# Optimization experiments

Measured on AMD Instinct MI355X. Metric: run time of the kernel, lower is better.

## Reference

```python
import jax, jax.numpy as jnp
import numpy as np


def setup_inputs() -> dict:
    key = jax.random.key(0)
    k1, k2, k3 = jax.random.split(key, 3)
    B, N, DK, DV = 8, 4096, 32, 32
    KEY = jax.random.normal(k1, (B, N, DK), dtype=jnp.float32)
    VALUE = jax.random.normal(k2, (B, N, DV), dtype=jnp.float32)
    QUERY = jax.random.normal(k3, (B, N, DK), dtype=jnp.float32)
    W = jnp.ones((DK,), dtype=jnp.float32)
    return {"KEY": KEY, "VALUE": VALUE, "QUERY": QUERY, "W": W}


def reference(KEY, VALUE, QUERY, W):
    # mads forward with type='nwd', kernel='gauss'
    ks = KEY * W            # (b, nk, d) scaled keys
    qs = QUERY * W          # (b, nq, d) scaled queries
    # squared euclidean distance via the gram trick (avoids b*nk*nq*d tensor)
    k2 = jnp.sum(ks * ks, axis=-1)                      # (b, nk)
    q2 = jnp.sum(qs * qs, axis=-1)                      # (b, nq)
    cross = jnp.einsum('bik,bjk->bij', ks, qs)          # (b, nk, nq)
    d2 = jnp.maximum(k2[:, :, None] + q2[:, None, :] - 2.0 * cross, 0.0)
    # gauss kernel: -dist^2 / 2, softmax over the key axis (dim=1)
    attn = jax.nn.softmax(-0.5 * d2, axis=1)            # (b, nk, nq)
    # weighted sum of values: (b, nk, nq) x (b, nk, dv) -> (b, nq, dv)
    out = jnp.einsum('bij,bik->bjk', attn, VALUE)
    return out
```

## Files before the change

kernel.cpp:

```cpp
#include <hip/hip_runtime.h>


#define L2E 1.4426950408889634f

typedef float f32x4 __attribute__((ext_vector_type(4)));
typedef short s16x8 __attribute__((ext_vector_type(8)));

__device__ __forceinline__ unsigned int f2bf(float f) {
    unsigned int u = __float_as_uint(f);
    return (u + 0x7FFFu + ((u >> 16) & 1u)) >> 16;
}
__device__ __forceinline__ float bf2f(unsigned int h) {
    return __uint_as_float(h << 16);
}
__device__ __forceinline__ float exp2_hw(float x) {
    float r;
    asm("v_exp_f32 %0, %1" : "=v"(r) : "v"(x));
    return r;
}
__device__ __forceinline__ unsigned int cvt_pk_bf16(float lo, float hi) {
    unsigned int r;
    asm("v_cvt_pk_bf16_f32 %0, %1, %2" : "=v"(r) : "v"(lo), "v"(hi));
    return r;
}

__global__ __launch_bounds__(256)
void prep_k_kernel(const float* __restrict__ K, const float* __restrict__ Wp,
                   unsigned short* __restrict__ KHI, unsigned short* __restrict__ KLO,
                   float* __restrict__ K2S)
{
    const size_t gtid = (size_t)blockIdx.x * 256 + threadIdx.x;
    const int row = (int)(gtid >> 3);
    const int c0  = ((int)gtid & 7) * 4;
    const float4 k = *(const float4*)(K + (size_t)row * 32 + c0);
    const float4 w = *(const float4*)(Wp + c0);
    float ks0 = k.x * w.x, ks1 = k.y * w.y, ks2 = k.z * w.z, ks3 = k.w * w.w;
    float pk = ks0 * ks0 + ks1 * ks1 + ks2 * ks2 + ks3 * ks3;
    pk += __shfl_xor(pk, 1);
    pk += __shfl_xor(pk, 2);
    pk += __shfl_xor(pk, 4);
    if (c0 == 0) K2S[row] = -0.5f * pk;
    unsigned int h0 = f2bf(ks0), h1 = f2bf(ks1), h2 = f2bf(ks2), h3 = f2bf(ks3);
    unsigned int l0 = f2bf(ks0 - bf2f(h0)), l1 = f2bf(ks1 - bf2f(h1));
    unsigned int l2 = f2bf(ks2 - bf2f(h2)), l3 = f2bf(ks3 - bf2f(h3));
    uint2 hp, lp;
    hp.x = h0 | (h1 << 16); hp.y = h2 | (h3 << 16);
    lp.x = l0 | (l1 << 16); lp.y = l2 | (l3 << 16);
    *(uint2*)(KHI + (size_t)row * 32 + c0) = hp;
    *(uint2*)(KLO + (size_t)row * 32 + c0) = lp;
}

__global__ __launch_bounds__(256)
void prep_v_kernel(const float* __restrict__ V, unsigned short* __restrict__ VT)
{
    __shared__ unsigned short tile[32][72];
    const int t  = threadIdx.x;
    const int b  = blockIdx.x >> 6;
    const int n0 = (blockIdx.x & 63) * 64;
    {
        const int nl = t >> 2, c0 = (t & 3) * 8;
        const float* vp = V + ((size_t)(b * 4096 + n0 + nl)) * 32 + c0;
        const float4 a = *(const float4*)vp;
        const float4 c = *(const float4*)(vp + 4);
        tile[c0 + 0][nl] = (unsigned short)f2bf(a.x);
        tile[c0 + 1][nl] = (unsigned short)f2bf(a.y);
        tile[c0 + 2][nl] = (unsigned short)f2bf(a.z);
        tile[c0 + 3][nl] = (unsigned short)f2bf(a.w);
        tile[c0 + 4][nl] = (unsigned short)f2bf(c.x);
        tile[c0 + 5][nl] = (unsigned short)f2bf(c.y);
        tile[c0 + 6][nl] = (unsigned short)f2bf(c.z);
        tile[c0 + 7][nl] = (unsigned short)f2bf(c.w);
    }
    __syncthreads();
    {
        const int v = t >> 3, ch = (t & 7) * 8;
        s16x8 o;
        #pragma unroll
        for (int j = 0; j < 8; ++j) o[j] = (short)tile[v][ch + j];
        *(s16x8*)(VT + ((size_t)(b * 32 + v)) * 4096 + n0 + ch) = o;
    }
}

__global__ __launch_bounds__(512, 4)
void mads_main_kernel(const unsigned short* __restrict__ KHI,
                      const unsigned short* __restrict__ KLO,
                      const unsigned short* __restrict__ VT,
                      const float* __restrict__ K2S,
                      const float* __restrict__ Q,
                      const float* __restrict__ Wp,
                      float* __restrict__ OUT)
{
    constexpr int N = 4096, D = 32;
    constexpr int NW = 8;
    constexpr int KPW = N / NW;
    constexpr int RND = KPW / 32;

    __shared__ __align__(16) unsigned int pbuf[NW][4][16][16];
    __shared__ float lbuf[NW][4][16];
    __shared__ float sumb[4][32][16];

    const int tid  = threadIdx.x;
    const int lane = tid & 63;
    const int w    = tid >> 6;
    const int g    = lane >> 4;
    const int qi   = lane & 15;
    const int b    = blockIdx.x & 7;
    const int q0   = (blockIdx.x >> 3) * 64;

    for (int i = tid; i < 4 * 32 * 16; i += 512) ((float*)sumb)[i] = 0.f;

    float w8[8];
    {
        const float* wp = Wp + g * 8;
        #pragma unroll
        for (int j = 0; j < 8; ++j) w8[j] = wp[j];
    }
    s16x8 qhi[4], qlo[4];
    float nq2L[4];
    #pragma unroll
    for (int sub = 0; sub < 4; ++sub) {
        const float* qp = Q + ((size_t)(b * N + q0 + sub * 16 + qi)) * D + g * 8;
        float s = 0.f;
        #pragma unroll
        for (int j = 0; j < 8; ++j) {
            float qs = qp[j] * w8[j];
            s = fmaf(qs, qs, s);
            unsigned int h = f2bf(qs);
            qhi[sub][j] = (short)h;
            qlo[sub][j] = (short)f2bf(qs - bf2f(h));
        }
        s += __shfl_xor(s, 16);
        s += __shfl_xor(s, 32);
        nq2L[sub] = -0.5f * s * L2E;
    }

    f32x4 acc[4][2];
    #pragma unroll
    for (int s = 0; s < 4; ++s)
        #pragma unroll
        for (int v = 0; v < 2; ++v)
            #pragma unroll
            for (int i = 0; i < 4; ++i) acc[s][v][i] = 0.f;

    float l_run[4] = {0.f, 0.f, 0.f, 0.f};

    const int pcr = (g + (qi >> 1)) & 3;

    for (int rnd = 0; rnd < RND; ++rnd) {
        const int kb = w * KPW + rnd * 32;

        const size_t krow = ((size_t)(b * N + kb + qi)) * 32 + g * 8;
        const s16x8 kh0 = *(const s16x8*)(KHI + krow);
        const s16x8 kh1 = *(const s16x8*)(KHI + krow + 16 * 32);
        const s16x8 kl0 = *(const s16x8*)(KLO + krow);
        const s16x8 kl1 = *(const s16x8*)(KLO + krow + 16 * 32);
        const f32x4 k2c0 = *(const f32x4*)(K2S + b * N + kb + g * 4);
        const f32x4 k2c1 = *(const f32x4*)(K2S + b * N + kb + 16 + g * 4);
        const s16x8 vf0 = *(const s16x8*)(VT + ((size_t)(b * 32 + qi)) * N + kb + g * 8);
        const s16x8 vf1 = *(const s16x8*)(VT + ((size_t)(b * 32 + 16 + qi)) * N + kb + g * 8);

        #pragma unroll
        for (int sub = 0; sub < 4; ++sub) {
            f32x4 sv[2];
            sv[0] = k2c0;
            sv[1] = k2c1;
            sv[0] = __builtin_amdgcn_mfma_f32_16x16x32_bf16(kl0, qhi[sub], sv[0], 0, 0, 0);
            sv[0] = __builtin_amdgcn_mfma_f32_16x16x32_bf16(kh0, qlo[sub], sv[0], 0, 0, 0);
            sv[0] = __builtin_amdgcn_mfma_f32_16x16x32_bf16(kh0, qhi[sub], sv[0], 0, 0, 0);
            sv[1] = __builtin_amdgcn_mfma_f32_16x16x32_bf16(kl1, qhi[sub], sv[1], 0, 0, 0);
            sv[1] = __builtin_amdgcn_mfma_f32_16x16x32_bf16(kh1, qlo[sub], sv[1], 0, 0, 0);
            sv[1] = __builtin_amdgcn_mfma_f32_16x16x32_bf16(kh1, qhi[sub], sv[1], 0, 0, 0);

            float p[8];
            #pragma unroll
            for (int kst = 0; kst < 2; ++kst)
                #pragma unroll
                for (int r = 0; r < 4; ++r)
                    p[kst * 4 + r] = exp2_hw(fmaf(sv[kst][r], L2E, nq2L[sub]));

            l_run[sub] += ((p[0] + p[1]) + (p[2] + p[3]))
                        + ((p[4] + p[5]) + (p[6] + p[7]));

            unsigned int pd[2][2];
            pd[0][0] = cvt_pk_bf16(p[0], p[1]);
            pd[0][1] = cvt_pk_bf16(p[2], p[3]);
            pd[1][0] = cvt_pk_bf16(p[4], p[5]);
            pd[1][1] = cvt_pk_bf16(p[6], p[7]);
            #pragma unroll
            for (int kst = 0; kst < 2; ++kst) {
                int c  = kst * 2 + (g >> 1);
                int pc = (c + (qi >> 1)) & 3;
                unsigned long long pack64 =
                    (unsigned long long)pd[kst][0] |
                    ((unsigned long long)pd[kst][1] << 32);
                *(unsigned long long*)&pbuf[w][sub][qi][pc * 4 + (g & 1) * 2] = pack64;
            }
        }

        #pragma unroll
        for (int sub = 0; sub < 4; ++sub) {
            s16x8 pf = *(const s16x8*)&pbuf[w][sub][qi][pcr * 4];
            acc[sub][0] = __builtin_amdgcn_mfma_f32_16x16x32_bf16(vf0, pf, acc[sub][0], 0, 0, 0);
            acc[sub][1] = __builtin_amdgcn_mfma_f32_16x16x32_bf16(vf1, pf, acc[sub][1], 0, 0, 0);
        }
    }

    #pragma unroll
    for (int sub = 0; sub < 4; ++sub) {
        float lv = l_run[sub];
        lv += __shfl_xor(lv, 16);
        lv += __shfl_xor(lv, 32);
        if (g == 0) lbuf[w][sub][qi] = lv;
    }
    __syncthreads();

    #pragma unroll
    for (int sub = 0; sub < 4; ++sub)
        #pragma unroll
        for (int vt = 0; vt < 2; ++vt)
            #pragma unroll
            for (int r = 0; r < 4; ++r)
                atomicAdd(&sumb[sub][vt * 16 + g * 4 + r][qi], acc[sub][vt][r]);
    __syncthreads();

    {
        const int sub = tid >> 7;
        const int q   = (tid >> 3) & 15;
        const int v0  = (tid & 7) * 4;
        float lt = 0.f;
        #pragma unroll
        for (int ww = 0; ww < NW; ++ww) lt += lbuf[ww][sub][q];
        const float inv = 1.0f / lt;
        float* op = OUT + ((size_t)(b * N + q0 + sub * 16 + q)) * D + v0;
        #pragma unroll
        for (int i = 0; i < 4; ++i) op[i] = sumb[sub][v0 + i][q] * inv;
    }
}

__global__ __launch_bounds__(256, 2)
void mads_fb_kernel(const float* __restrict__ K,
                    const float* __restrict__ V,
                    const float* __restrict__ Q,
                    const float* __restrict__ Wp,
                    float* __restrict__ OUT)
{
    constexpr int N  = 4096, D = 32;
    constexpr int NW = 4;
    constexpr int KPW = N / NW;
    constexpr int RND = KPW / 32;

    __shared__ __align__(16) unsigned int pbuf[NW][4][16][16];
    __shared__ float mlbuf[NW][4][16][2];
    __shared__ float sumb[4][32][16];

    const int tid  = threadIdx.x;
    const int lane = tid & 63;
    const int w    = tid >> 6;
    const int g    = lane >> 4;
    const int qi   = lane & 15;
    const int b    = blockIdx.x >> 6;
    const int q0   = (blockIdx.x & 63) * 64;

    for (int i = tid; i < 4 * 32 * 16; i += 256) ((float*)sumb)[i] = 0.f;

    float w8[8];
    {
        const float* wp = Wp + g * 8;
        #pragma unroll
        for (int j = 0; j < 8; ++j) w8[j] = wp[j];
    }

    s16x8 qhi[4], qlo[4];
    #pragma unroll
    for (int sub = 0; sub < 4; ++sub) {
        const float* qp = Q + ((size_t)(b * N + q0 + sub * 16 + qi)) * D + g * 8;
        #pragma unroll
        for (int j = 0; j < 8; ++j) {
            float qs = qp[j] * w8[j];
            unsigned int h = f2bf(qs);
            qhi[sub][j] = (short)h;
            qlo[sub][j] = (short)f2bf(qs - bf2f(h));
        }
    }

    f32x4 acc[4][2];
    #pragma unroll
    for (int s = 0; s < 4; ++s)
        #pragma unroll
        for (int v = 0; v < 2; ++v)
            #pragma unroll
            for (int i = 0; i < 4; ++i) acc[s][v][i] = 0.f;

    float m_run[4] = {-1e30f, -1e30f, -1e30f, -1e30f};
    float l_run[4] = {0.f, 0.f, 0.f, 0.f};

    for (int rnd = 0; rnd < RND; ++rnd) {
        const int kb = w * KPW + rnd * 32;

        float kraw[2][8], vraw[2][8];
        #pragma unroll
        for (int kst = 0; kst < 2; ++kst) {
            const float* kp = K + ((size_t)(b * N + kb + kst * 16 + qi)) * D + g * 8;
            #pragma unroll
            for (int j = 0; j < 8; ++j) kraw[kst][j] = kp[j];
        }
        #pragma unroll
        for (int vt = 0; vt < 2; ++vt) {
            const float* vp = V + ((size_t)(b * N + kb + g * 8)) * D + vt * 16 + qi;
            #pragma unroll
            for (int j = 0; j < 8; ++j) vraw[vt][j] = vp[(size_t)j * D];
        }

        s16x8 khi[2], klo[2];
        f32x4 k2c[2];
        #pragma unroll
        for (int kst = 0; kst < 2; ++kst) {
            float pk = 0.f;
            #pragma unroll
            for (int j = 0; j < 8; ++j) {
                float ks = kraw[kst][j] * w8[j];
                pk = fmaf(ks, ks, pk);
                unsigned int h = f2bf(ks);
                khi[kst][j] = (short)h;
                klo[kst][j] = (short)f2bf(ks - bf2f(h));
            }
            pk += __shfl_xor(pk, 16);
            pk += __shfl_xor(pk, 32);
            pk *= -0.5f;
            #pragma unroll
            for (int r = 0; r < 4; ++r)
                k2c[kst][r] = __shfl(pk, ((lane >> 4) << 2) + r);
        }

        #pragma unroll
        for (int sub = 0; sub < 4; ++sub) {
            f32x4 sv[2];
            sv[0] = k2c[0];
            sv[1] = k2c[1];
            sv[0] = __builtin_amdgcn_mfma_f32_16x16x32_bf16(klo[0], qhi[sub], sv[0], 0, 0, 0);
            sv[0] = __builtin_amdgcn_mfma_f32_16x16x32_bf16(khi[0], qlo[sub], sv[0], 0, 0, 0);
            sv[0] = __builtin_amdgcn_mfma_f32_16x16x32_bf16(khi[0], qhi[sub], sv[0], 0, 0, 0);
            sv[1] = __builtin_amdgcn_mfma_f32_16x16x32_bf16(klo[1], qhi[sub], sv[1], 0, 0, 0);
            sv[1] = __builtin_amdgcn_mfma_f32_16x16x32_bf16(khi[1], qlo[sub], sv[1], 0, 0, 0);
            sv[1] = __builtin_amdgcn_mfma_f32_16x16x32_bf16(khi[1], qhi[sub], sv[1], 0, 0, 0);

            float tm = sv[0][0];
            tm = fmaxf(tm, sv[0][1]); tm = fmaxf(tm, sv[0][2]); tm = fmaxf(tm, sv[0][3]);
            tm = fmaxf(tm, sv[1][0]); tm = fmaxf(tm, sv[1][1]);
            tm = fmaxf(tm, sv[1][2]); tm = fmaxf(tm, sv[1][3]);
            tm = fmaxf(tm, __shfl_xor(tm, 16));
            tm = fmaxf(tm, __shfl_xor(tm, 32));

            float mnew  = fmaxf(m_run[sub], tm);
            float scale = exp2_hw((m_run[sub] - mnew) * L2E);
            m_run[sub]  = mnew;
            float nmL   = -mnew * L2E;

            acc[sub][0] *= scale;
            acc[sub][1] *= scale;

            float ps = 0.f;
            unsigned int pd[2][2];
            #pragma unroll
            for (int kst = 0; kst < 2; ++kst) {
                float p[4];
                #pragma unroll
                for (int r = 0; r < 4; ++r) {
                    p[r] = exp2_hw(fmaf(sv[kst][r], L2E, nmL));
                    ps += p[r];
                }
                pd[kst][0] = f2bf(p[0]) | (f2bf(p[1]) << 16);
                pd[kst][1] = f2bf(p[2]) | (f2bf(p[3]) << 16);
            }
            l_run[sub] = l_run[sub] * scale + ps;

            #pragma unroll
            for (int kst = 0; kst < 2; ++kst) {
                int c  = kst * 2 + (g >> 1);
                int pc = (c + (qi >> 1)) & 3;
                unsigned long long pack64 =
                    (unsigned long long)pd[kst][0] |
                    ((unsigned long long)pd[kst][1] << 32);
                *(unsigned long long*)&pbuf[w][sub][qi][pc * 4 + (g & 1) * 2] = pack64;
            }
        }

        s16x8 vfr[2];
        #pragma unroll
        for (int vt = 0; vt < 2; ++vt)
            #pragma unroll
            for (int j = 0; j < 8; ++j) vfr[vt][j] = (short)f2bf(vraw[vt][j]);

        const int pcr = (g + (qi >> 1)) & 3;
        #pragma unroll
        for (int sub = 0; sub < 4; ++sub) {
            s16x8 pf = *(const s16x8*)&pbuf[w][sub][qi][pcr * 4];
            acc[sub][0] = __builtin_amdgcn_mfma_f32_16x16x32_bf16(vfr[0], pf, acc[sub][0], 0, 0, 0);
            acc[sub][1] = __builtin_amdgcn_mfma_f32_16x16x32_bf16(vfr[1], pf, acc[sub][1], 0, 0, 0);
        }
    }

    #pragma unroll
    for (int sub = 0; sub < 4; ++sub) {
        float lv = l_run[sub];
        lv += __shfl_xor(lv, 16);
        lv += __shfl_xor(lv, 32);
        l_run[sub] = lv;
    }
    if (g == 0) {
        #pragma unroll
        for (int sub = 0; sub < 4; ++sub) {
            mlbuf[w][sub][qi][0] = m_run[sub];
            mlbuf[w][sub][qi][1] = l_run[sub];
        }
    }
    __syncthreads();

    #pragma unroll
    for (int sub = 0; sub < 4; ++sub) {
        float M = -1e30f;
        float mv[NW], lv[NW];
        #pragma unroll
        for (int ww = 0; ww < NW; ++ww) {
            mv[ww] = mlbuf[ww][sub][qi][0];
            lv[ww] = mlbuf[ww][sub][qi][1];
            M = fmaxf(M, mv[ww]);
        }
        float denom = 0.f;
        #pragma unroll
        for (int ww = 0; ww < NW; ++ww)
            denom += lv[ww] * exp2_hw((mv[ww] - M) * L2E);
        float sc = exp2_hw((m_run[sub] - M) * L2E) / denom;
        #pragma unroll
        for (int vt = 0; vt < 2; ++vt)
            #pragma unroll
            for (int r = 0; r < 4; ++r)
                atomicAdd(&sumb[sub][vt * 16 + g * 4 + r][qi], acc[sub][vt][r] * sc);
    }
    __syncthreads();

    {
        const int sub = tid >> 6;
        const int q   = (tid >> 2) & 15;
        const int v0  = (tid & 3) * 8;
        float* op = OUT + ((size_t)(b * N + q0 + sub * 16 + q)) * D + v0;
        #pragma unroll
        for (int i = 0; i < 8; ++i) op[i] = sumb[sub][v0 + i][q];
    }
}

extern "C" void kernel_launch(void* const* d_in, const int* in_sizes, int n_in,
                              void* d_out, int out_size, void* d_ws, size_t ws_size,
                              hipStream_t stream) {
    const float* K  = (const float*)d_in[0];
    const float* V  = (const float*)d_in[1];
    const float* Q  = (const float*)d_in[2];
    const float* W  = (const float*)d_in[3];
    float* OUT = (float*)d_out;
    (void)in_sizes; (void)n_in; (void)out_size;

    constexpr size_t NEL = (size_t)8 * 4096 * 32;
    constexpr size_t NROW = (size_t)8 * 4096;
    constexpr size_t NEED_MONO = NEL * 2 * 3 + NROW * 4;

    if (ws_size >= NEED_MONO) {
        unsigned short* khi = (unsigned short*)d_ws;
        unsigned short* klo = khi + NEL;
        unsigned short* vt  = klo + NEL;
        float*          k2s = (float*)(vt + NEL);
        hipLaunchKernelGGL(prep_k_kernel, dim3(1024), dim3(256), 0, stream, K, W, khi, klo, k2s);
        hipLaunchKernelGGL(prep_v_kernel, dim3(512),  dim3(256), 0, stream, V, vt);
        hipLaunchKernelGGL(mads_main_kernel, dim3(512), dim3(512), 0, stream,
                           khi, klo, vt, k2s, Q, W, OUT);
    } else {
        hipLaunchKernelGGL(mads_fb_kernel, dim3(512), dim3(256), 0, stream,
                           K, V, Q, W, OUT);
    }
}
```

Measured before the change: 95.70 us.

## Pre-pack K/V fragments in MFMA order and double-buffer via global_load_lds

Replaces the separate K hi/lo and transposed V prep kernels with one pack kernel that writes, per 32-key tile, the exact per-lane MFMA fragment layout (K hi/lo halves and V columns) as contiguous 512-element blocks. The main kernel streams these tiles into per-wave LDS double buffers with asynchronous global_load_lds and explicit vmcnt waits, prefetching the next tile while computing on the current one. The goal is to hide global load latency and make fragment loads fully coalesced. In exchange it uses more LDS, and launch bounds drop from 4 to 2 blocks per CU, which may lower occupancy. The pack kernel also does strided V reads.

```diff
diff --git a/kernel.cpp b/kernel.cpp
--- a/kernel.cpp
+++ b/kernel.cpp
@@ -25,9 +25,8 @@
 }
 
 __global__ __launch_bounds__(256)
-void prep_k_kernel(const float* __restrict__ K, const float* __restrict__ Wp,
-                   unsigned short* __restrict__ KHI, unsigned short* __restrict__ KLO,
-                   float* __restrict__ K2S)
+void prep_k2_kernel(const float* __restrict__ K, const float* __restrict__ Wp,
+                    float* __restrict__ K2S)
 {
     const size_t gtid = (size_t)blockIdx.x * 256 + threadIdx.x;
     const int row = (int)(gtid >> 3);
@@ -40,51 +39,46 @@
     pk += __shfl_xor(pk, 2);
     pk += __shfl_xor(pk, 4);
     if (c0 == 0) K2S[row] = -0.5f * pk;
-    unsigned int h0 = f2bf(ks0), h1 = f2bf(ks1), h2 = f2bf(ks2), h3 = f2bf(ks3);
-    unsigned int l0 = f2bf(ks0 - bf2f(h0)), l1 = f2bf(ks1 - bf2f(h1));
-    unsigned int l2 = f2bf(ks2 - bf2f(h2)), l3 = f2bf(ks3 - bf2f(h3));
-    uint2 hp, lp;
-    hp.x = h0 | (h1 << 16); hp.y = h2 | (h3 << 16);
-    lp.x = l0 | (l1 << 16); lp.y = l2 | (l3 << 16);
-    *(uint2*)(KHI + (size_t)row * 32 + c0) = hp;
-    *(uint2*)(KLO + (size_t)row * 32 + c0) = lp;
 }
 
 __global__ __launch_bounds__(256)
-void prep_v_kernel(const float* __restrict__ V, unsigned short* __restrict__ VT)
+void prep_pack_kernel(const float* __restrict__ K, const float* __restrict__ V,
+                      const float* __restrict__ Wp, unsigned short* __restrict__ PKS)
 {
-    __shared__ unsigned short tile[32][72];
-    const int t  = threadIdx.x;
-    const int b  = blockIdx.x >> 6;
-    const int n0 = (blockIdx.x & 63) * 64;
-    {
-        const int nl = t >> 2, c0 = (t & 3) * 8;
-        const float* vp = V + ((size_t)(b * 4096 + n0 + nl)) * 32 + c0;
-        const float4 a = *(const float4*)vp;
-        const float4 c = *(const float4*)(vp + 4);
-        tile[c0 + 0][nl] = (unsigned short)f2bf(a.x);
-        tile[c0 + 1][nl] = (unsigned short)f2bf(a.y);
-        tile[c0 + 2][nl] = (unsigned short)f2bf(a.z);
-        tile[c0 + 3][nl] = (unsigned short)f2bf(a.w);
-        tile[c0 + 4][nl] = (unsigned short)f2bf(c.x);
-        tile[c0 + 5][nl] = (unsigned short)f2bf(c.y);
-        tile[c0 + 6][nl] = (unsigned short)f2bf(c.z);
-        tile[c0 + 7][nl] = (unsigned short)f2bf(c.w);
-    }
-    __syncthreads();
-    {
-        const int v = t >> 3, ch = (t & 7) * 8;
-        s16x8 o;
-        #pragma unroll
-        for (int j = 0; j < 8; ++j) o[j] = (short)tile[v][ch + j];
-        *(s16x8*)(VT + ((size_t)(b * 32 + v)) * 4096 + n0 + ch) = o;
-    }
-}
-
-__global__ __launch_bounds__(512, 4)
-void mads_main_kernel(const unsigned short* __restrict__ KHI,
-                      const unsigned short* __restrict__ KLO,
-                      const unsigned short* __restrict__ VT,
+    const size_t gtid = (size_t)blockIdx.x * 256 + threadIdx.x;
+    const int lane = (int)(gtid & 63);
+    const int tmp  = (int)(gtid >> 6);
+    const int i    = tmp % 6;
+    const int tmp2 = tmp / 6;
+    const int t    = tmp2 & 127;
+    const int b    = tmp2 >> 7;
+    const int qi   = lane & 15;
+    const int g    = lane >> 4;
+
+    s16x8 o;
+    if (i < 4) {
+        const int key = t * 32 + ((i & 1) ? 16 : 0) + qi;
+        const int d0  = g * 8;
+        const float* kp = K + ((size_t)(b * 4096 + key)) * 32 + d0;
+        const float* wp = Wp + d0;
+        #pragma unroll
+        for (int j = 0; j < 8; ++j) {
+            float ks = kp[j] * wp[j];
+            unsigned int h = f2bf(ks);
+            o[j] = (i < 2) ? (short)h : (short)f2bf(ks - bf2f(h));
+        }
+    } else {
+        const int v  = ((i == 5) ? 16 : 0) + qi;
+        const int k0 = t * 32 + g * 8;
+        const float* vp = V + ((size_t)(b * 4096 + k0)) * 32 + v;
+        #pragma unroll
+        for (int j = 0; j < 8; ++j) o[j] = (short)f2bf(vp[(size_t)j * 32]);
+    }
+    *(s16x8*)(PKS + gtid * 8) = o;
+}
+
+__global__ __launch_bounds__(512, 2)
+void mads_main_kernel(const unsigned short* __restrict__ PKS,
                       const float* __restrict__ K2S,
                       const float* __restrict__ Q,
                       const float* __restrict__ Wp,
@@ -92,9 +86,9 @@
 {
     constexpr int N = 4096, D = 32;
     constexpr int NW = 8;
-    constexpr int KPW = N / NW;
-    constexpr int RND = KPW / 32;
-
+    constexpr int TPW = 16;
+
+    __shared__ __align__(16) unsigned short stg[NW][2][6][512];
     __shared__ __align__(16) unsigned int pbuf[NW][4][16][16];
     __shared__ float lbuf[NW][4][16];
     __shared__ float sumb[4][32][16];
@@ -143,21 +137,41 @@
             for (int i = 0; i < 4; ++i) acc[s][v][i] = 0.f;
 
     float l_run[4] = {0.f, 0.f, 0.f, 0.f};
-
     const int pcr = (g + (qi >> 1)) & 3;
-
-    for (int rnd = 0; rnd < RND; ++rnd) {
-        const int kb = w * KPW + rnd * 32;
-
-        const size_t krow = ((size_t)(b * N + kb + qi)) * 32 + g * 8;
-        const s16x8 kh0 = *(const s16x8*)(KHI + krow);
-        const s16x8 kh1 = *(const s16x8*)(KHI + krow + 16 * 32);
-        const s16x8 kl0 = *(const s16x8*)(KLO + krow);
-        const s16x8 kl1 = *(const s16x8*)(KLO + krow + 16 * 32);
+    const int tbase = w * TPW;
+
+    const unsigned short* pks_base = PKS + ((size_t)(b * 128 + tbase) * 6) * 512 + lane * 8;
+
+    auto stage = [&](int buf, int t) {
+        const unsigned short* gp = pks_base + (size_t)t * 6 * 512;
+        #pragma unroll
+        for (int i = 0; i < 6; ++i)
+            __builtin_amdgcn_global_load_lds((const void*)(gp + i * 512),
+                                             (void*)&stg[w][buf][i][0], 16, 0, 0);
+    };
+
+    stage(0, 0);
+
+    for (int rnd = 0; rnd < TPW; ++rnd) {
+        const int cur = rnd & 1;
+        const int kb  = (tbase + rnd) * 32;
+
         const f32x4 k2c0 = *(const f32x4*)(K2S + b * N + kb + g * 4);
         const f32x4 k2c1 = *(const f32x4*)(K2S + b * N + kb + 16 + g * 4);
-        const s16x8 vf0 = *(const s16x8*)(VT + ((size_t)(b * 32 + qi)) * N + kb + g * 8);
-        const s16x8 vf1 = *(const s16x8*)(VT + ((size_t)(b * 32 + 16 + qi)) * N + kb + g * 8);
+
+        if (rnd < TPW - 1) {
+            stage(cur ^ 1, rnd + 1);
+            asm volatile("s_waitcnt vmcnt(6)" ::: "memory");
+        } else {
+            asm volatile("s_waitcnt vmcnt(0)" ::: "memory");
+        }
+
+        const s16x8 kh0 = *(const s16x8*)&stg[w][cur][0][lane * 8];
+        const s16x8 kh1 = *(const s16x8*)&stg[w][cur][1][lane * 8];
+        const s16x8 kl0 = *(const s16x8*)&stg[w][cur][2][lane * 8];
+        const s16x8 kl1 = *(const s16x8*)&stg[w][cur][3][lane * 8];
+        const s16x8 vf0 = *(const s16x8*)&stg[w][cur][4][lane * 8];
+        const s16x8 vf1 = *(const s16x8*)&stg[w][cur][5][lane * 8];
 
         #pragma unroll
         for (int sub = 0; sub < 4; ++sub) {
@@ -459,19 +473,17 @@
     float* OUT = (float*)d_out;
     (void)in_sizes; (void)n_in; (void)out_size;
 
-    constexpr size_t NEL = (size_t)8 * 4096 * 32;
-    constexpr size_t NROW = (size_t)8 * 4096;
-    constexpr size_t NEED_MONO = NEL * 2 * 3 + NROW * 4;
-
-    if (ws_size >= NEED_MONO) {
-        unsigned short* khi = (unsigned short*)d_ws;
-        unsigned short* klo = khi + NEL;
-        unsigned short* vt  = klo + NEL;
-        float*          k2s = (float*)(vt + NEL);
-        hipLaunchKernelGGL(prep_k_kernel, dim3(1024), dim3(256), 0, stream, K, W, khi, klo, k2s);
-        hipLaunchKernelGGL(prep_v_kernel, dim3(512),  dim3(256), 0, stream, V, vt);
-        hipLaunchKernelGGL(mads_main_kernel, dim3(512), dim3(512), 0, stream,
-                           khi, klo, vt, k2s, Q, W, OUT);
+    constexpr size_t PKS_EL = (size_t)8 * 128 * 6 * 512;
+    constexpr size_t NROW   = (size_t)8 * 4096;
+    constexpr size_t NEED   = PKS_EL * 2 + NROW * 4;
+
+    if (ws_size >= NEED) {
+        unsigned short* pks = (unsigned short*)d_ws;
+        float*          k2s = (float*)(pks + PKS_EL);
+        hipLaunchKernelGGL(prep_k2_kernel,   dim3(1024), dim3(256), 0, stream, K, W, k2s);
+        hipLaunchKernelGGL(prep_pack_kernel, dim3(1536), dim3(256), 0, stream, K, V, W, pks);
+        hipLaunchKernelGGL(mads_main_kernel, dim3(512),  dim3(512), 0, stream,
+                           pks, k2s, Q, W, OUT);
     } else {
         hipLaunchKernelGGL(mads_fb_kernel, dim3(512), dim3(256), 0, stream,
                            K, V, Q, W, OUT);
```

After: 106.6 us. 11.4% more time.
